# Optimization experiments

Measured on AMD Instinct MI355X. Metric: run time of the kernel, lower is better.

Reference implementation:

```python
import jax, jax.numpy as jnp
import numpy as np

D = 1024
H = 16
HD = D // H
FF = 4096
B = 2
S = 2048


def _layer_norm(x, g, b, eps=1e-5):
    mu = jnp.mean(x, axis=-1, keepdims=True)
    var = jnp.mean(jnp.square(x - mu), axis=-1, keepdims=True)
    return (x - mu) * jax.lax.rsqrt(var + eps) * g + b


def setup_inputs() -> dict:
    key = jax.random.key(0)
    ks = jax.random.split(key, 16)
    s = 0.02
    return {
        "x": jax.random.normal(ks[0], (B, S, D), jnp.float32),
        "Wq": jax.random.normal(ks[1], (H, D, HD), jnp.float32) * s,
        "bq": jnp.zeros((H, HD), jnp.float32),
        "Wk": jax.random.normal(ks[2], (H, D, HD), jnp.float32) * s,
        "bk": jnp.zeros((H, HD), jnp.float32),
        "Wv": jax.random.normal(ks[3], (H, D, HD), jnp.float32) * s,
        "bv": jnp.zeros((H, HD), jnp.float32),
        "Wo": jax.random.normal(ks[4], (D, D), jnp.float32) * s,
        "bo": jnp.zeros((D,), jnp.float32),
        "W1": jax.random.normal(ks[5], (D, FF), jnp.float32) * s,
        "b1": jnp.zeros((FF,), jnp.float32),
        "W2": jax.random.normal(ks[6], (FF, D), jnp.float32) * s,
        "b2": jnp.zeros((D,), jnp.float32),
        "g1": jnp.ones((D,), jnp.float32),
        "be1": jnp.zeros((D,), jnp.float32),
        "g2": jnp.ones((D,), jnp.float32),
        "be2": jnp.zeros((D,), jnp.float32),
    }


def reference(x, Wq, bq, Wk, bk, Wv, bv, Wo, bo, W1, b1, W2, b2, g1, be1, g2, be2):
    b, s, d = x.shape
    # per-head projections (vectorized over heads)
    q = jnp.einsum("bsd,hde->bhse", x, Wq) + bq[None, :, None, :]
    k = jnp.einsum("bsd,hde->bhse", x, Wk) + bk[None, :, None, :]
    v = jnp.einsum("bsd,hde->bhse", x, Wv) + bv[None, :, None, :]
    # NOTE: source scales by 1/dim_k (not 1/sqrt(dim_k)) -- kept faithful
    scores = jnp.einsum("bhse,bhte->bhst", q, k) / jnp.asarray(HD, x.dtype)
    causal = jnp.tril(jnp.ones((s, s), bool))  # [S,S]
    scores = jnp.where(causal[None, None], scores, jnp.asarray(-jnp.inf, x.dtype))
    attn = jax.nn.softmax(scores, axis=-1)
    ctx = jnp.einsum("bhst,bhte->bhse", attn, v)  # [B,H,S,hd]
    ctx = jnp.transpose(ctx, (0, 2, 1, 3)).reshape(b, s, d)  # concat heads
    attn_out = ctx @ Wo + bo
    x = _layer_norm(x + attn_out, g1, be1)
    # feed-forward: linear -> exact GELU -> linear (dropout = eval identity)
    h = jax.nn.gelu(x @ W1 + b1, approximate=False)
    ff = h @ W2 + b2
    return _layer_norm(x + ff, g2, be2)
```

## Files before the change

kernel.cpp:

```cpp
#include <hip/hip_runtime.h>
#include <math.h>

constexpr int Dm  = 1024;
constexpr int Hh  = 16;
constexpr int HDm = 64;
constexpr int FFm = 4096;
constexpr int Bb  = 2;
constexpr int Sq  = 2048;
constexpr int Mm  = Bb * Sq;

typedef __attribute__((ext_vector_type(8))) short short8;
typedef __attribute__((ext_vector_type(4))) short short4v;
typedef __attribute__((ext_vector_type(4))) float f32x4;

#define AS1 __attribute__((address_space(1)))
#define AS3 __attribute__((address_space(3)))

constexpr float QSCALE = 0.022542110013890054f;

__device__ __forceinline__ unsigned short f2b(float f) {
    union { float f; unsigned u; } v; v.f = f;
    unsigned r = v.u + 0x7FFFu + ((v.u >> 16) & 1u);
    return (unsigned short)(r >> 16);
}

__global__ __launch_bounds__(256) void convert_x(const float* __restrict__ x,
                                                 short* __restrict__ xb) {
    int i = blockIdx.x * 256 + threadIdx.x;
    float4 v = ((const float4*)x)[i];
    short4v o;
    o[0] = (short)f2b(v.x); o[1] = (short)f2b(v.y);
    o[2] = (short)f2b(v.z); o[3] = (short)f2b(v.w);
    ((short4v*)xb)[i] = o;
}

__global__ __launch_bounds__(256) void transpose_to_bf16(
    const float* __restrict__ src, short* __restrict__ dst, int R, int C) {
    __shared__ float t[64][65];
    const int c0 = blockIdx.x * 64, r0 = blockIdx.y * 64;
    const int lc = threadIdx.x & 63, lr4 = threadIdx.x >> 6;
    #pragma unroll
    for (int p = 0; p < 16; ++p) {
        int rr = p * 4 + lr4;
        t[rr][lc] = src[(size_t)(r0 + rr) * C + c0 + lc];
    }
    __syncthreads();
    #pragma unroll
    for (int p = 0; p < 16; ++p) {
        int rr = p * 4 + lr4;
        dst[(size_t)(c0 + rr) * R + r0 + lc] = (short)f2b(t[lc][rr]);
    }
}

__global__ __launch_bounds__(256) void build_wqkv(
    const float* __restrict__ Wq, const float* __restrict__ Wk,
    const float* __restrict__ Wv, short* __restrict__ dst) {
    const int kt = blockIdx.x, h = blockIdx.y, which = blockIdx.z;
    const float* W = ((which == 0) ? Wq : (which == 1) ? Wk : Wv) +
                     (size_t)h * Dm * HDm;
    __shared__ float t[64][65];
    const int lc = threadIdx.x & 63, lr4 = threadIdx.x >> 6;
    #pragma unroll
    for (int p = 0; p < 16; ++p) {
        int kr = p * 4 + lr4;
        t[kr][lc] = W[(size_t)(kt * 64 + kr) * HDm + lc];
    }
    __syncthreads();
    const int nbase = which * 1024 + h * 64;
    #pragma unroll
    for (int p = 0; p < 16; ++p) {
        int e = p * 4 + lr4;
        dst[(size_t)(nbase + e) * Dm + kt * 64 + lc] = (short)f2b(t[lc][e]);
    }
}

__global__ __launch_bounds__(256) void build_bqkv(
    const float* __restrict__ bq, const float* __restrict__ bk,
    const float* __restrict__ bv, float* __restrict__ bcat) {
    int n = blockIdx.x * 256 + threadIdx.x;
    const float* s = (n < 1024) ? bq : (n < 2048) ? bk : bv;
    bcat[n] = s[n & 1023];
}

__global__ __launch_bounds__(256) void transpose_v(
    const short* __restrict__ v, short* __restrict__ vt)
{
    const int st = blockIdx.x;
    const int h = blockIdx.y & 15, b = blockIdx.y >> 4;
    __shared__ short t[64][72];
    const int tid = threadIdx.x;
    const size_t base = ((size_t)b * Hh + h) * Sq * HDm;
    #pragma unroll
    for (int r = 0; r < 2; ++r) {
        int c = tid + 256 * r;
        int srow = c >> 3, sch = c & 7;
        *(short8*)&t[srow][sch * 8] =
            *(const short8*)(v + base + (size_t)(st * 64 + srow) * HDm + sch * 8);
    }
    __syncthreads();
    const size_t obase = ((size_t)b * Hh + h) * HDm * Sq;
    #pragma unroll
    for (int r = 0; r < 2; ++r) {
        int c = tid + 256 * r;
        int erow = c >> 3, sch = c & 7;
        short8 o8;
        #pragma unroll
        for (int j = 0; j < 8; ++j) o8[j] = t[sch * 8 + j][erow];
        *(short8*)(vt + obase + (size_t)erow * Sq + st * 64 + sch * 8) = o8;
    }
}

template<int EPI>
__global__ __launch_bounds__(512, 2) void gemm256(
    const short* __restrict__ A, const short* __restrict__ Bt,
    const float* __restrict__ bias,
    short* __restrict__ outb,
    short* __restrict__ qo, short* __restrict__ ko, short* __restrict__ vo,
    int K, int N, int NMT)
{
    __shared__ __align__(16) char lds[131072];
    char* const ldsA = lds;
    char* const ldsB = lds + 65536;
    const int tid = threadIdx.x;
    const int l = tid & 63, wv = tid >> 6;
    const int wm = wv >> 2, wn = wv & 3;
    const int lr = l & 15, lg = l >> 4;
    const int bid = blockIdx.x;
    const int m0 = (bid % NMT) * 256;
    const int n0 = (bid / NMT) * 256;
    const size_t KB = (size_t)K * 2;
    const int NT = K >> 6;

    const char* pA[2][2];
    const char* pB[2][2];
    #pragma unroll
    for (int i = 0; i < 2; ++i) {
        int c = tid + 512 * i;
        int rh = c >> 3, j = c & 7;
        int sw = (j ^ (rh & 7)) << 4;
        #pragma unroll
        for (int h = 0; h < 2; ++h) {
            pA[h][i] = (const char*)A + (size_t)(m0 + h * 128 + rh) * KB + sw;
            pB[h][i] = (const char*)Bt + (size_t)(n0 + h * 128 + rh) * KB + sw;
        }
    }
    const int dbase = tid * 16;

    f32x4 acc[8][4];
    f32x4 z4 = {0.f, 0.f, 0.f, 0.f};
    #pragma unroll
    for (int i = 0; i < 8; ++i)
        #pragma unroll
        for (int j = 0; j < 4; ++j) acc[i][j] = z4;

#define STAGE_B(h, nb) do {                                                     \
    char* _b = ldsB + ((nb) * 2 + (h)) * 16384;                                 \
    __builtin_amdgcn_global_load_lds((const AS1 void*)pB[h][0],                 \
        (AS3 void*)(_b + dbase), 16, 0, 0);                                     \
    __builtin_amdgcn_global_load_lds((const AS1 void*)pB[h][1],                 \
        (AS3 void*)(_b + dbase + 8192), 16, 0, 0);                              \
    pB[h][0] += 128; pB[h][1] += 128; } while (0)
#define STAGE_A(h, nb) do {                                                     \
    char* _a = ldsA + ((nb) * 2 + (h)) * 16384;                                 \
    __builtin_amdgcn_global_load_lds((const AS1 void*)pA[h][0],                 \
        (AS3 void*)(_a + dbase), 16, 0, 0);                                     \
    __builtin_amdgcn_global_load_lds((const AS1 void*)pA[h][1],                 \
        (AS3 void*)(_a + dbase + 8192), 16, 0, 0);                              \
    pA[h][0] += 128; pA[h][1] += 128; } while (0)

    STAGE_B(0, 0); STAGE_B(1, 0); STAGE_A(0, 0); STAGE_A(1, 0);
    asm volatile("s_waitcnt vmcnt(2)" ::: "memory");
    __builtin_amdgcn_s_barrier();
    __builtin_amdgcn_sched_barrier(0);

    const int swk0 = ((0 + lg) ^ (lr & 7)) << 4;
    const int swk1 = ((4 + lg) ^ (lr & 7)) << 4;

    for (int kt = 0; kt < NT; ++kt) {
        const int buf = kt & 1, nbuf = buf ^ 1;
        const bool more = (kt + 1 < NT);
        char* const Ah0 = ldsA + (buf * 2) * 16384;
        char* const Ah1 = ldsA + (buf * 2 + 1) * 16384;
        char* const Bh  = ldsB + (buf * 2 + (wn >> 1)) * 16384 + (wn & 1) * 8192;

        short8 bf[4][2];
        #pragma unroll
        for (int nf = 0; nf < 4; ++nf) {
            const char* bb = Bh + (nf * 16 + lr) * 128;
            bf[nf][0] = *(const short8*)(bb + swk0);
            bf[nf][1] = *(const short8*)(bb + swk1);
        }
        short8 af[2][2];

#define LOAD_A(p) do {                                                          \
    _Pragma("unroll")                                                           \
    for (int j2 = 0; j2 < 2; ++j2) {                                            \
        const int mf = 2 * (p) + j2;                                            \
        const char* ab = ((mf >> 2) ? Ah1 : Ah0) +                              \
                         ((mf & 3) * 32 + wm * 16 + lr) * 128;                  \
        af[j2][0] = *(const short8*)(ab + swk0);                                \
        af[j2][1] = *(const short8*)(ab + swk1);                                \
    } } while (0)

#define MFMA8(p) do {                                                           \
    _Pragma("unroll")                                                           \
    for (int j2 = 0; j2 < 2; ++j2)                                              \
        _Pragma("unroll")                                                       \
        for (int nf = 0; nf < 4; ++nf) {                                        \
            acc[2 * (p) + j2][nf] = __builtin_amdgcn_mfma_f32_16x16x32_bf16(    \
                af[j2][0], bf[nf][0], acc[2 * (p) + j2][nf], 0, 0, 0);          \
            acc[2 * (p) + j2][nf] = __builtin_amdgcn_mfma_f32_16x16x32_bf16(    \
                af[j2][1], bf[nf][1], acc[2 * (p) + j2][nf], 0, 0, 0);          \
        } } while (0)

        LOAD_A(0);
        if (more) STAGE_B(0, nbuf);
        __builtin_amdgcn_s_barrier();
        asm volatile("s_waitcnt lgkmcnt(0)" ::: "memory");
        __builtin_amdgcn_sched_barrier(0);
        __builtin_amdgcn_s_setprio(1);
        MFMA8(0);
        __builtin_amdgcn_s_setprio(0);
        __builtin_amdgcn_s_barrier();
        LOAD_A(1);
        if (more) STAGE_B(1, nbuf);
        __builtin_amdgcn_s_barrier();
        asm volatile("s_waitcnt lgkmcnt(0)" ::: "memory");
        __builtin_amdgcn_sched_barrier(0);
        __builtin_amdgcn_s_setprio(1);
        MFMA8(1);
        __builtin_amdgcn_s_setprio(0);
        if (more) asm volatile("s_waitcnt vmcnt(4)" ::: "memory");
        else      asm volatile("s_waitcnt vmcnt(0)" ::: "memory");
        __builtin_amdgcn_s_barrier();
        __builtin_amdgcn_sched_barrier(0);
        LOAD_A(2);
        if (more) STAGE_A(0, nbuf);
        __builtin_amdgcn_s_barrier();
        asm volatile("s_waitcnt lgkmcnt(0)" ::: "memory");
        __builtin_amdgcn_sched_barrier(0);
        __builtin_amdgcn_s_setprio(1);
        MFMA8(2);
        __builtin_amdgcn_s_setprio(0);
        __builtin_amdgcn_s_barrier();
        LOAD_A(3);
        if (more) STAGE_A(1, nbuf);
        __builtin_amdgcn_s_barrier();
        asm volatile("s_waitcnt lgkmcnt(0)" ::: "memory");
        __builtin_amdgcn_sched_barrier(0);
        __builtin_amdgcn_s_setprio(1);
        MFMA8(3);
        __builtin_amdgcn_s_setprio(0);
        asm volatile("s_waitcnt vmcnt(2)" ::: "memory");
        __builtin_amdgcn_s_barrier();
        __builtin_amdgcn_sched_barrier(0);
#undef LOAD_A
#undef MFMA8
    }

    #pragma unroll
    for (int mf = 0; mf < 8; ++mf) {
        #pragma unroll
        for (int nf = 0; nf < 4; ++nf) {
            #pragma unroll
            for (int r = 0; r < 4; ++r) {
                int m = m0 + mf * 32 + wm * 16 + lg * 4 + r;
                int n = n0 + wn * 64 + nf * 16 + lr;
                float val = acc[mf][nf][r] + bias[n];
                if (EPI == 1) {
                    val = 0.5f * val * (1.0f + erff(val * 0.70710678118654752f));
                    outb[(size_t)m * N + n] = (short)f2b(val);
                } else {
                    int which = n >> 10, hh = (n >> 6) & 15, e = n & 63;
                    if (which == 0) val *= QSCALE;
                    int bb2 = m >> 11, ss = m & 2047;
                    short* o = (which == 0) ? qo : (which == 1) ? ko : vo;
                    o[(((size_t)bb2 * Hh + hh) * Sq + ss) * HDm + e] = (short)f2b(val);
                }
            }
        }
    }
#undef STAGE_A
#undef STAGE_B
}

template<int EPI, int BM>
__global__ __launch_bounds__(256) void gemm_bf16(
    const short* __restrict__ A, const short* __restrict__ Bt,
    const float* __restrict__ bias, const float* __restrict__ res,
    float* __restrict__ outf, short* __restrict__ outb,
    int K, int N)
{
    constexpr int BMW = BM / 2;
    constexpr int MF  = BMW / 16;
    __shared__ __align__(16) char smem[BM * 128 + 16384];
    char* ldsA = smem;
    char* ldsB = smem + BM * 128;
    const int tid = threadIdx.x;
    const int l = tid & 63, wv = tid >> 6;
    const int wr = wv >> 1, wc = wv & 1, lr = l & 15, lg = l >> 4;
    const int m0 = blockIdx.x * BM, n0 = blockIdx.y * 128;
    const size_t KB = (size_t)K * 2;
    const char* Ab = (const char*)A;
    const char* Bb = (const char*)Bt;

    f32x4 zero4 = {0.f, 0.f, 0.f, 0.f};
    f32x4 acc[MF][4];
    #pragma unroll
    for (int i = 0; i < MF; ++i)
        #pragma unroll
        for (int j = 0; j < 4; ++j) acc[i][j] = zero4;

    for (int k0 = 0; k0 < K; k0 += 64) {
        __syncthreads();
        #pragma unroll
        for (int r = 0; r < BM / 32; ++r) {
            int c  = (wv * (BM / 32) + r) * 64;
            int cl = c + l;
            int row = cl >> 3, j = cl & 7;
            int sw = ((j ^ (row & 7)) << 4);
            __builtin_amdgcn_global_load_lds(
                (const AS1 void*)(Ab + (size_t)(m0 + row) * KB + (size_t)k0 * 2 + sw),
                (AS3 void*)(ldsA + c * 16), 16, 0, 0);
        }
        #pragma unroll
        for (int r = 0; r < 4; ++r) {
            int c  = (wv * 4 + r) * 64;
            int cl = c + l;
            int row = cl >> 3, j = cl & 7;
            int sw = ((j ^ (row & 7)) << 4);
            __builtin_amdgcn_global_load_lds(
                (const AS1 void*)(Bb + (size_t)(n0 + row) * KB + (size_t)k0 * 2 + sw),
                (AS3 void*)(ldsB + c * 16), 16, 0, 0);
        }
        __syncthreads();
        #pragma unroll
        for (int ks = 0; ks < 2; ++ks) {
            short8 af[MF], bf[4];
            #pragma unroll
            for (int i = 0; i < MF; ++i) {
                int rowA = wr * BMW + i * 16 + lr;
                af[i] = *(const short8*)(ldsA + rowA * 128 +
                            (((ks * 4 + lg) ^ (rowA & 7)) << 4));
            }
            #pragma unroll
            for (int i = 0; i < 4; ++i) {
                int rowB = wc * 64 + i * 16 + lr;
                bf[i] = *(const short8*)(ldsB + rowB * 128 +
                            (((ks * 4 + lg) ^ (rowB & 7)) << 4));
            }
            #pragma unroll
            for (int i = 0; i < MF; ++i)
                #pragma unroll
                for (int jn = 0; jn < 4; ++jn)
                    acc[i][jn] = __builtin_amdgcn_mfma_f32_16x16x32_bf16(
                        af[i], bf[jn], acc[i][jn], 0, 0, 0);
        }
    }

    #pragma unroll
    for (int i = 0; i < MF; ++i) {
        #pragma unroll
        for (int jn = 0; jn < 4; ++jn) {
            #pragma unroll
            for (int r = 0; r < 4; ++r) {
                int m = m0 + wr * BMW + i * 16 + lg * 4 + r;
                int n = n0 + wc * 64 + jn * 16 + lr;
                float val = acc[i][jn][r];
                if (EPI == 0) {
                    val += bias[n] + res[(size_t)m * N + n];
                    outf[(size_t)m * N + n] = val;
                } else {
                    val += bias[n];
                    val = 0.5f * val * (1.0f + erff(val * 0.70710678118654752f));
                    outb[(size_t)m * N + n] = (short)f2b(val);
                }
            }
        }
    }
}

__global__ __launch_bounds__(256) void attn_mfma(
    const short* __restrict__ qg, const short* __restrict__ kg,
    const short* __restrict__ vtg, short* __restrict__ ctx)
{
    const int bid = blockIdx.x;
    const int qt = (Sq / 64 - 1) - (bid >> 5);
    const int hb = bid & 31;
    const int h = hb & 15, b = hb >> 4;
    const int tid = threadIdx.x;
    const int l = tid & 63, wv = tid >> 6;
    const int lr = l & 15, lg = l >> 4;

    __shared__ __align__(16) char KlB[8192];
    __shared__ __align__(16) char VtB[8192];
    __shared__ __align__(16) char PlB[4][2048];

    const size_t bh = ((size_t)b * Hh + h) * Sq;
    const size_t vbase = ((size_t)b * Hh + h) * HDm * Sq;

    const int qbase = qt * 64 + wv * 16;
    short8 aq[2];
    #pragma unroll
    for (int ks = 0; ks < 2; ++ks)
        aq[ks] = *(const short8*)(qg + (bh + qbase + lr) * HDm + ks * 32 + lg * 8);

    f32x4 zero4 = {0.f, 0.f, 0.f, 0.f};
    f32x4 oacc[4], lacc = zero4;
    #pragma unroll
    for (int i = 0; i < 4; ++i) oacc[i] = zero4;
    float mreg[4];
    #pragma unroll
    for (int r = 0; r < 4; ++r) mreg[r] = -3e38f;

    short8 vone;
    #pragma unroll
    for (int j = 0; j < 8; ++j) vone[j] = (short)0x3F80;

    char* plw = PlB[wv];

    const char* srcK[2]; const char* srcV[2];
    #pragma unroll
    for (int r2 = 0; r2 < 2; ++r2) {
        int cl = tid + 256 * r2;
        int row = cl >> 3, j = cl & 7;
        srcK[r2] = (const char*)kg + ((bh + row) * HDm + ((j ^ (row & 7)) * 8)) * 2;
        srcV[r2] = (const char*)vtg + (vbase + (size_t)row * Sq + ((j ^ (row & 7)) * 8)) * 2;
    }

    const int nt = qt + 1;
    for (int tk = 0; tk < nt; ++tk) {
        __syncthreads();
        #pragma unroll
        for (int r2 = 0; r2 < 2; ++r2) {
            int c = tid + 256 * r2;
            __builtin_amdgcn_global_load_lds((const AS1 void*)srcK[r2],
                (AS3 void*)(KlB + c * 16), 16, 0, 0);
            srcK[r2] += 64 * HDm * 2;
            __builtin_amdgcn_global_load_lds((const AS1 void*)srcV[r2],
                (AS3 void*)(VtB + c * 16), 16, 0, 0);
            srcV[r2] += 64 * 2;
        }
        __syncthreads();

        f32x4 sc[4];
        #pragma unroll
        for (int i = 0; i < 4; ++i) sc[i] = zero4;
        __builtin_amdgcn_s_setprio(1);
        #pragma unroll
        for (int kd = 0; kd < 2; ++kd) {
            #pragma unroll
            for (int nf = 0; nf < 4; ++nf) {
                short8 bk = *(const short8*)(KlB + (nf * 16 + lr) * 128 +
                                (((kd * 4 + lg) ^ (lr & 7)) << 4));
                sc[nf] = __builtin_amdgcn_mfma_f32_16x16x32_bf16(
                    aq[kd], bk, sc[nf], 0, 0, 0);
            }
        }
        __builtin_amdgcn_s_setprio(0);

        const bool dm = (tk == qt);
        float mrow[4];
        #pragma unroll
        for (int r = 0; r < 4; ++r) {
            const int qglob = qbase + lg * 4 + r;
            if (dm) {
                #pragma unroll
                for (int nf = 0; nf < 4; ++nf)
                    if (tk * 64 + nf * 16 + lr > qglob) sc[nf][r] = -3e38f;
            }
            float mr = fmaxf(fmaxf(sc[0][r], sc[1][r]), fmaxf(sc[2][r], sc[3][r]));
            #pragma unroll
            for (int o = 1; o < 16; o <<= 1)
                mr = fmaxf(mr, __shfl_xor(mr, o));
            mrow[r] = mr;
        }

        bool grow = (mrow[0] > mreg[0] + 8.f) || (mrow[1] > mreg[1] + 8.f) ||
                    (mrow[2] > mreg[2] + 8.f) || (mrow[3] > mreg[3] + 8.f);
        if (__any((int)grow)) {
            #pragma unroll
            for (int r = 0; r < 4; ++r) {
                float mnew = fmaxf(mreg[r], mrow[r]);
                float cf = exp2f(mreg[r] - mnew);
                mreg[r] = mnew;
                const int prow = lg * 4 + r;
                #pragma unroll
                for (int nf = 0; nf < 4; ++nf) {
                    float p = exp2f(sc[nf][r] - mnew);
                    *(unsigned short*)(plw + prow * 128 +
                        (((nf * 2 + (lr >> 3)) ^ (prow & 7)) << 4) +
                        ((lr & 7) << 1)) = (unsigned short)(__float_as_uint(p) >> 16);
                }
                #pragma unroll
                for (int nf = 0; nf < 4; ++nf) oacc[nf][r] *= cf;
                lacc[r] *= cf;
            }
        } else {
            #pragma unroll
            for (int r = 0; r < 4; ++r) {
                const int prow = lg * 4 + r;
                #pragma unroll
                for (int nf = 0; nf < 4; ++nf) {
                    float p = exp2f(sc[nf][r] - mreg[r]);
                    *(unsigned short*)(plw + prow * 128 +
                        (((nf * 2 + (lr >> 3)) ^ (prow & 7)) << 4) +
                        ((lr & 7) << 1)) = (unsigned short)(__float_as_uint(p) >> 16);
                }
            }
        }

        asm volatile("s_waitcnt lgkmcnt(0)" ::: "memory");
        __builtin_amdgcn_sched_barrier(0);

        __builtin_amdgcn_s_setprio(1);
        #pragma unroll
        for (int ks = 0; ks < 2; ++ks) {
            short8 pa = *(const short8*)(plw + lr * 128 +
                            (((ks * 4 + lg) ^ (lr & 7)) << 4));
            #pragma unroll
            for (int nf = 0; nf < 4; ++nf) {
                short8 bv8 = *(const short8*)(VtB + (nf * 16 + lr) * 128 +
                                (((ks * 4 + lg) ^ (lr & 7)) << 4));
                oacc[nf] = __builtin_amdgcn_mfma_f32_16x16x32_bf16(
                    pa, bv8, oacc[nf], 0, 0, 0);
            }
            lacc = __builtin_amdgcn_mfma_f32_16x16x32_bf16(pa, vone, lacc, 0, 0, 0);
        }
        __builtin_amdgcn_s_setprio(0);
    }

    #pragma unroll
    for (int r = 0; r < 4; ++r) {
        float inv = 1.0f / lacc[r];
        int q = qbase + lg * 4 + r;
        size_t o = ((size_t)b * Sq + q) * Dm + h * HDm;
        #pragma unroll
        for (int nf = 0; nf < 4; ++nf)
            ctx[o + nf * 16 + lr] = (short)f2b(oacc[nf][r] * inv);
    }
}

template<int BF16OUT>
__global__ __launch_bounds__(256) void ln_kernel(
    const float* __restrict__ in, const float* __restrict__ g,
    const float* __restrict__ be, float* __restrict__ outf,
    short* __restrict__ outb)
{
    const int m = blockIdx.x;
    const int tid = threadIdx.x;
    const float4 vl = *(const float4*)&in[(size_t)m * Dm + tid * 4];
    float s  = vl.x + vl.y + vl.z + vl.w;
    float s2 = vl.x * vl.x + vl.y * vl.y + vl.z * vl.z + vl.w * vl.w;
    #pragma unroll
    for (int o = 32; o > 0; o >>= 1) {
        s  += __shfl_down(s, o);
        s2 += __shfl_down(s2, o);
    }
    __shared__ float rs[4], rs2[4];
    const int w = tid >> 6;
    if ((tid & 63) == 0) { rs[w] = s; rs2[w] = s2; }
    __syncthreads();
    s  = rs[0] + rs[1] + rs[2] + rs[3];
    s2 = rs2[0] + rs2[1] + rs2[2] + rs2[3];
    const float mean = s * (1.0f / Dm);
    const float var  = s2 * (1.0f / Dm) - mean * mean;
    const float rstd = rsqrtf(var + 1e-5f);
    const float4 gv = *(const float4*)&g[tid * 4];
    const float4 bv = *(const float4*)&be[tid * 4];
    float4 ov;
    ov.x = (vl.x - mean) * rstd * gv.x + bv.x;
    ov.y = (vl.y - mean) * rstd * gv.y + bv.y;
    ov.z = (vl.z - mean) * rstd * gv.z + bv.z;
    ov.w = (vl.w - mean) * rstd * gv.w + bv.w;
    *(float4*)&outf[(size_t)m * Dm + tid * 4] = ov;
    if (BF16OUT) {
        short4v o4;
        o4[0] = (short)f2b(ov.x); o4[1] = (short)f2b(ov.y);
        o4[2] = (short)f2b(ov.z); o4[3] = (short)f2b(ov.w);
        *(short4v*)&outb[(size_t)m * Dm + tid * 4] = o4;
    }
}

extern "C" void kernel_launch(void* const* d_in, const int* in_sizes, int n_in,
                              void* d_out, int out_size, void* d_ws, size_t ws_size,
                              hipStream_t stream)
{
    const float* x  = (const float*)d_in[0];
    const float* Wq = (const float*)d_in[1];
    const float* bq = (const float*)d_in[2];
    const float* Wk = (const float*)d_in[3];
    const float* bk = (const float*)d_in[4];
    const float* Wv = (const float*)d_in[5];
    const float* bv = (const float*)d_in[6];
    const float* Wo = (const float*)d_in[7];
    const float* bo = (const float*)d_in[8];
    const float* W1 = (const float*)d_in[9];
    const float* b1 = (const float*)d_in[10];
    const float* W2 = (const float*)d_in[11];
    const float* b2 = (const float*)d_in[12];
    const float* g1 = (const float*)d_in[13];
    const float* be1= (const float*)d_in[14];
    const float* g2 = (const float*)d_in[15];
    const float* be2= (const float*)d_in[16];
    float* out = (float*)d_out;

    char* ws = (char*)d_ws;
    size_t off = 0;
    auto alloc = [&](size_t bytes) {
        char* p = ws + off;
        off += (bytes + 255) & ~(size_t)255;
        return p;
    };
    const size_t MD2 = (size_t)Mm * Dm * 2;
    short* xb    = (short*)alloc(MD2);
    short* wqkvt = (short*)alloc((size_t)3072 * Dm * 2);
    float* bcat  = (float*)alloc(3072 * 4);
    short* wot   = (short*)alloc((size_t)Dm * Dm * 2);
    short* w1t   = (short*)alloc((size_t)FFm * Dm * 2);
    short* w2t   = (short*)alloc((size_t)Dm * FFm * 2);
    short* qb    = (short*)alloc(MD2);
    short* kb    = (short*)alloc(MD2);
    short* vb    = (short*)alloc(MD2);
    short* ctxb  = (short*)alloc(MD2);
    short* hb    = qb;
    float* y     = (float*)alloc((size_t)Mm * Dm * 4);
    float* x1f   = (float*)alloc((size_t)Mm * Dm * 4);
    short* x1b   = (short*)alloc(MD2);
    float* y2    = y;
    short* vtb   = (short*)y;

    convert_x<<<Mm * Dm / 1024, 256, 0, stream>>>(x, xb);
    build_wqkv<<<dim3(16, 16, 3), 256, 0, stream>>>(Wq, Wk, Wv, wqkvt);
    build_bqkv<<<12, 256, 0, stream>>>(bq, bk, bv, bcat);
    transpose_to_bf16<<<dim3(16, 16), 256, 0, stream>>>(Wo, wot, Dm, Dm);
    transpose_to_bf16<<<dim3(64, 16), 256, 0, stream>>>(W1, w1t, Dm, FFm);
    transpose_to_bf16<<<dim3(16, 64), 256, 0, stream>>>(W2, w2t, FFm, Dm);

    gemm256<2><<<192, 512, 0, stream>>>(
        xb, wqkvt, bcat, nullptr, qb, kb, vb, Dm, 3072, 16);
    transpose_v<<<dim3(32, 32), 256, 0, stream>>>(vb, vtb);
    attn_mfma<<<1024, 256, 0, stream>>>(qb, kb, vtb, ctxb);
    gemm_bf16<0, 64><<<dim3(64, 8), 256, 0, stream>>>(
        ctxb, wot, bo, x, y, nullptr, Dm, Dm);
    ln_kernel<1><<<Mm, 256, 0, stream>>>(y, g1, be1, x1f, x1b);
    gemm256<1><<<256, 512, 0, stream>>>(
        x1b, w1t, b1, hb, nullptr, nullptr, nullptr, Dm, FFm, 16);
    gemm_bf16<0, 64><<<dim3(64, 8), 256, 0, stream>>>(
        hb, w2t, b2, x1f, y2, nullptr, FFm, Dm);
    ln_kernel<0><<<Mm, 256, 0, stream>>>(y2, g2, be2, out, nullptr);
}
```

Before: 264.7 us.

## Load attention K/V fragments straight into registers instead of shared memory

Each wave in the attention kernel now loads its own K and V^T MFMA operand fragments from global memory into registers. This replaces the block-cooperative global_load_lds staging and drops the two __syncthreads per key tile. The next tile's K is prefetched during the softmax phase, and the row-max shuffle reduction now runs only when the rescale path is taken. The trade-off is that each of the 4 waves fetches the same K/V separately (4x more global/L2 traffic), and register pressure goes up.

Result: slower. 336.9 us (+27.3%).

```diff
diff --git a/kernel.cpp b/kernel.cpp
--- a/kernel.cpp
+++ b/kernel.cpp
@@ -392,9 +392,8 @@
     const int l = tid & 63, wv = tid >> 6;
     const int lr = l & 15, lg = l >> 4;
 
-    __shared__ __align__(16) char KlB[8192];
-    __shared__ __align__(16) char VtB[8192];
     __shared__ __align__(16) char PlB[4][2048];
+    char* plw = PlB[wv];
 
     const size_t bh = ((size_t)b * Hh + h) * Sq;
     const size_t vbase = ((size_t)b * Hh + h) * HDm * Sq;
@@ -417,71 +416,63 @@
     #pragma unroll
     for (int j = 0; j < 8; ++j) vone[j] = (short)0x3F80;
 
-    char* plw = PlB[wv];
-
-    const char* srcK[2]; const char* srcV[2];
-    #pragma unroll
-    for (int r2 = 0; r2 < 2; ++r2) {
-        int cl = tid + 256 * r2;
-        int row = cl >> 3, j = cl & 7;
-        srcK[r2] = (const char*)kg + ((bh + row) * HDm + ((j ^ (row & 7)) * 8)) * 2;
-        srcV[r2] = (const char*)vtg + (vbase + (size_t)row * Sq + ((j ^ (row & 7)) * 8)) * 2;
-    }
+    const char* kp = (const char*)kg + ((bh + lr) * HDm + lg * 8) * 2;
+    const char* vp = (const char*)vtg + (vbase + (size_t)lr * Sq + lg * 8) * 2;
+
+    short8 kf[2][4], vf[2][4];
+    #pragma unroll
+    for (int kd = 0; kd < 2; ++kd)
+        #pragma unroll
+        for (int nf = 0; nf < 4; ++nf)
+            kf[kd][nf] = *(const short8*)(kp + nf * 2048 + kd * 64);
+    kp += 8192;
 
     const int nt = qt + 1;
     for (int tk = 0; tk < nt; ++tk) {
-        __syncthreads();
-        #pragma unroll
-        for (int r2 = 0; r2 < 2; ++r2) {
-            int c = tid + 256 * r2;
-            __builtin_amdgcn_global_load_lds((const AS1 void*)srcK[r2],
-                (AS3 void*)(KlB + c * 16), 16, 0, 0);
-            srcK[r2] += 64 * HDm * 2;
-            __builtin_amdgcn_global_load_lds((const AS1 void*)srcV[r2],
-                (AS3 void*)(VtB + c * 16), 16, 0, 0);
-            srcV[r2] += 64 * 2;
-        }
-        __syncthreads();
+        #pragma unroll
+        for (int ks = 0; ks < 2; ++ks)
+            #pragma unroll
+            for (int nf = 0; nf < 4; ++nf)
+                vf[ks][nf] = *(const short8*)(vp + nf * (Sq * 32) + ks * 64);
+        vp += 128;
 
         f32x4 sc[4];
         #pragma unroll
         for (int i = 0; i < 4; ++i) sc[i] = zero4;
         __builtin_amdgcn_s_setprio(1);
         #pragma unroll
-        for (int kd = 0; kd < 2; ++kd) {
-            #pragma unroll
-            for (int nf = 0; nf < 4; ++nf) {
-                short8 bk = *(const short8*)(KlB + (nf * 16 + lr) * 128 +
-                                (((kd * 4 + lg) ^ (lr & 7)) << 4));
+        for (int kd = 0; kd < 2; ++kd)
+            #pragma unroll
+            for (int nf = 0; nf < 4; ++nf)
                 sc[nf] = __builtin_amdgcn_mfma_f32_16x16x32_bf16(
-                    aq[kd], bk, sc[nf], 0, 0, 0);
-            }
-        }
+                    aq[kd], kf[kd][nf], sc[nf], 0, 0, 0);
         __builtin_amdgcn_s_setprio(0);
 
-        const bool dm = (tk == qt);
-        float mrow[4];
-        #pragma unroll
-        for (int r = 0; r < 4; ++r) {
-            const int qglob = qbase + lg * 4 + r;
-            if (dm) {
+        if (tk == qt) {
+            #pragma unroll
+            for (int r = 0; r < 4; ++r) {
+                const int qglob = qbase + lg * 4 + r;
                 #pragma unroll
                 for (int nf = 0; nf < 4; ++nf)
                     if (tk * 64 + nf * 16 + lr > qglob) sc[nf][r] = -3e38f;
             }
-            float mr = fmaxf(fmaxf(sc[0][r], sc[1][r]), fmaxf(sc[2][r], sc[3][r]));
-            #pragma unroll
-            for (int o = 1; o < 16; o <<= 1)
-                mr = fmaxf(mr, __shfl_xor(mr, o));
-            mrow[r] = mr;
-        }
-
-        bool grow = (mrow[0] > mreg[0] + 8.f) || (mrow[1] > mreg[1] + 8.f) ||
-                    (mrow[2] > mreg[2] + 8.f) || (mrow[3] > mreg[3] + 8.f);
+        }
+
+        float lm[4];
+        #pragma unroll
+        for (int r = 0; r < 4; ++r)
+            lm[r] = fmaxf(fmaxf(sc[0][r], sc[1][r]), fmaxf(sc[2][r], sc[3][r]));
+        bool grow = (lm[0] > mreg[0] + 8.f) || (lm[1] > mreg[1] + 8.f) ||
+                    (lm[2] > mreg[2] + 8.f) || (lm[3] > mreg[3] + 8.f);
+
         if (__any((int)grow)) {
             #pragma unroll
             for (int r = 0; r < 4; ++r) {
-                float mnew = fmaxf(mreg[r], mrow[r]);
+                float mr = lm[r];
+                #pragma unroll
+                for (int o = 1; o < 16; o <<= 1)
+                    mr = fmaxf(mr, __shfl_xor(mr, o));
+                float mnew = fmaxf(mreg[r], mr);
                 float cf = exp2f(mreg[r] - mnew);
                 mreg[r] = mnew;
                 const int prow = lg * 4 + r;
@@ -510,6 +501,15 @@
             }
         }
 
+        if (tk + 1 < nt) {
+            #pragma unroll
+            for (int kd = 0; kd < 2; ++kd)
+                #pragma unroll
+                for (int nf = 0; nf < 4; ++nf)
+                    kf[kd][nf] = *(const short8*)(kp + nf * 2048 + kd * 64);
+            kp += 8192;
+        }
+
         asm volatile("s_waitcnt lgkmcnt(0)" ::: "memory");
         __builtin_amdgcn_sched_barrier(0);
 
@@ -519,12 +519,9 @@
             short8 pa = *(const short8*)(plw + lr * 128 +
                             (((ks * 4 + lg) ^ (lr & 7)) << 4));
             #pragma unroll
-            for (int nf = 0; nf < 4; ++nf) {
-                short8 bv8 = *(const short8*)(VtB + (nf * 16 + lr) * 128 +
-                                (((ks * 4 + lg) ^ (lr & 7)) << 4));
+            for (int nf = 0; nf < 4; ++nf)
                 oacc[nf] = __builtin_amdgcn_mfma_f32_16x16x32_bf16(
-                    pa, bv8, oacc[nf], 0, 0, 0);
-            }
+                    pa, vf[ks][nf], oacc[nf], 0, 0, 0);
             lacc = __builtin_amdgcn_mfma_f32_16x16x32_bf16(pa, vone, lacc, 0, 0, 0);
         }
         __builtin_amdgcn_s_setprio(0);
```

## Fuse V transpose into QKV GEMM epilogue and defer row-max shuffles

Applied to the files above, without the earlier changes.

The QKV projection epilogue now writes V directly in transposed [b,h,e,s] layout using packed 4-element stores, which removes the separate transpose_v kernel and its extra global round trip. The attention kernel now computes per-lane local maxima for its lazy-rescale check and only performs the cross-lane shuffle reduction when a rescale is actually triggered. This trims shuffle work on the common path. The V buffer gets its own allocation instead of aliasing y.

Measured after the change: 255.6 us. -3.5%, faster.

```diff
diff --git a/kernel.cpp b/kernel.cpp
--- a/kernel.cpp
+++ b/kernel.cpp
@@ -80,34 +80,6 @@
     int n = blockIdx.x * 256 + threadIdx.x;
     const float* s = (n < 1024) ? bq : (n < 2048) ? bk : bv;
     bcat[n] = s[n & 1023];
-}
-
-__global__ __launch_bounds__(256) void transpose_v(
-    const short* __restrict__ v, short* __restrict__ vt)
-{
-    const int st = blockIdx.x;
-    const int h = blockIdx.y & 15, b = blockIdx.y >> 4;
-    __shared__ short t[64][72];
-    const int tid = threadIdx.x;
-    const size_t base = ((size_t)b * Hh + h) * Sq * HDm;
-    #pragma unroll
-    for (int r = 0; r < 2; ++r) {
-        int c = tid + 256 * r;
-        int srow = c >> 3, sch = c & 7;
-        *(short8*)&t[srow][sch * 8] =
-            *(const short8*)(v + base + (size_t)(st * 64 + srow) * HDm + sch * 8);
-    }
-    __syncthreads();
-    const size_t obase = ((size_t)b * Hh + h) * HDm * Sq;
-    #pragma unroll
-    for (int r = 0; r < 2; ++r) {
-        int c = tid + 256 * r;
-        int erow = c >> 3, sch = c & 7;
-        short8 o8;
-        #pragma unroll
-        for (int j = 0; j < 8; ++j) o8[j] = t[sch * 8 + j][erow];
-        *(short8*)(vt + obase + (size_t)erow * Sq + st * 64 + sch * 8) = o8;
-    }
 }
 
 template<int EPI>
@@ -262,20 +234,32 @@
     for (int mf = 0; mf < 8; ++mf) {
         #pragma unroll
         for (int nf = 0; nf < 4; ++nf) {
-            #pragma unroll
-            for (int r = 0; r < 4; ++r) {
-                int m = m0 + mf * 32 + wm * 16 + lg * 4 + r;
-                int n = n0 + wn * 64 + nf * 16 + lr;
-                float val = acc[mf][nf][r] + bias[n];
-                if (EPI == 1) {
+            const int n = n0 + wn * 64 + nf * 16 + lr;
+            const int mB = m0 + mf * 32 + wm * 16 + lg * 4;
+            if (EPI == 1) {
+                #pragma unroll
+                for (int r = 0; r < 4; ++r) {
+                    float val = acc[mf][nf][r] + bias[n];
                     val = 0.5f * val * (1.0f + erff(val * 0.70710678118654752f));
-                    outb[(size_t)m * N + n] = (short)f2b(val);
+                    outb[(size_t)(mB + r) * N + n] = (short)f2b(val);
+                }
+            } else {
+                const int which = n >> 10, hh = (n >> 6) & 15, e = n & 63;
+                const int bb2 = mB >> 11, ss = mB & 2047;
+                if (which == 2) {
+                    short4v pk;
+                    #pragma unroll
+                    for (int r = 0; r < 4; ++r)
+                        pk[r] = (short)f2b(acc[mf][nf][r] + bias[n]);
+                    *(short4v*)&vo[(((size_t)bb2 * Hh + hh) * HDm + e) * Sq + ss] = pk;
                 } else {
-                    int which = n >> 10, hh = (n >> 6) & 15, e = n & 63;
-                    if (which == 0) val *= QSCALE;
-                    int bb2 = m >> 11, ss = m & 2047;
-                    short* o = (which == 0) ? qo : (which == 1) ? ko : vo;
-                    o[(((size_t)bb2 * Hh + hh) * Sq + ss) * HDm + e] = (short)f2b(val);
+                    short* o = (which == 0) ? qo : ko;
+                    const float sc = (which == 0) ? QSCALE : 1.0f;
+                    #pragma unroll
+                    for (int r = 0; r < 4; ++r) {
+                        float val = (acc[mf][nf][r] + bias[n]) * sc;
+                        o[(((size_t)bb2 * Hh + hh) * Sq + ss + r) * HDm + e] = (short)f2b(val);
+                    }
                 }
             }
         }
@@ -459,29 +443,31 @@
         }
         __builtin_amdgcn_s_setprio(0);
 
-        const bool dm = (tk == qt);
-        float mrow[4];
-        #pragma unroll
-        for (int r = 0; r < 4; ++r) {
-            const int qglob = qbase + lg * 4 + r;
-            if (dm) {
+        if (tk == qt) {
+            #pragma unroll
+            for (int r = 0; r < 4; ++r) {
+                const int qglob = qbase + lg * 4 + r;
                 #pragma unroll
                 for (int nf = 0; nf < 4; ++nf)
                     if (tk * 64 + nf * 16 + lr > qglob) sc[nf][r] = -3e38f;
             }
-            float mr = fmaxf(fmaxf(sc[0][r], sc[1][r]), fmaxf(sc[2][r], sc[3][r]));
-            #pragma unroll
-            for (int o = 1; o < 16; o <<= 1)
-                mr = fmaxf(mr, __shfl_xor(mr, o));
-            mrow[r] = mr;
-        }
-
-        bool grow = (mrow[0] > mreg[0] + 8.f) || (mrow[1] > mreg[1] + 8.f) ||
-                    (mrow[2] > mreg[2] + 8.f) || (mrow[3] > mreg[3] + 8.f);
+        }
+
+        float lm[4];
+        #pragma unroll
+        for (int r = 0; r < 4; ++r)
+            lm[r] = fmaxf(fmaxf(sc[0][r], sc[1][r]), fmaxf(sc[2][r], sc[3][r]));
+        bool grow = (lm[0] > mreg[0] + 8.f) || (lm[1] > mreg[1] + 8.f) ||
+                    (lm[2] > mreg[2] + 8.f) || (lm[3] > mreg[3] + 8.f);
+
         if (__any((int)grow)) {
             #pragma unroll
             for (int r = 0; r < 4; ++r) {
-                float mnew = fmaxf(mreg[r], mrow[r]);
+                float mr = lm[r];
+                #pragma unroll
+                for (int o = 1; o < 16; o <<= 1)
+                    mr = fmaxf(mr, __shfl_xor(mr, o));
+                float mnew = fmaxf(mreg[r], mr);
                 float cf = exp2f(mreg[r] - mnew);
                 mreg[r] = mnew;
                 const int prow = lg * 4 + r;
@@ -621,14 +607,13 @@
     short* w2t   = (short*)alloc((size_t)Dm * FFm * 2);
     short* qb    = (short*)alloc(MD2);
     short* kb    = (short*)alloc(MD2);
-    short* vb    = (short*)alloc(MD2);
+    short* vtb   = (short*)alloc(MD2);
     short* ctxb  = (short*)alloc(MD2);
     short* hb    = qb;
     float* y     = (float*)alloc((size_t)Mm * Dm * 4);
     float* x1f   = (float*)alloc((size_t)Mm * Dm * 4);
     short* x1b   = (short*)alloc(MD2);
     float* y2    = y;
-    short* vtb   = (short*)y;
 
     convert_x<<<Mm * Dm / 1024, 256, 0, stream>>>(x, xb);
     build_wqkv<<<dim3(16, 16, 3), 256, 0, stream>>>(Wq, Wk, Wv, wqkvt);
@@ -638,8 +623,7 @@
     transpose_to_bf16<<<dim3(16, 64), 256, 0, stream>>>(W2, w2t, FFm, Dm);
 
     gemm256<2><<<192, 512, 0, stream>>>(
-        xb, wqkvt, bcat, nullptr, qb, kb, vb, Dm, 3072, 16);
-    transpose_v<<<dim3(32, 32), 256, 0, stream>>>(vb, vtb);
+        xb, wqkvt, bcat, nullptr, qb, kb, vtb, Dm, 3072, 16);
     attn_mfma<<<1024, 256, 0, stream>>>(qb, kb, vtb, ctxb);
     gemm_bf16<0, 64><<<dim3(64, 8), 256, 0, stream>>>(
         ctxb, wot, bo, x, y, nullptr, Dm, Dm);
```
